# Performance work log

Measured on AMD Instinct MI355X. Metric: run time of the kernel, lower is better.

The kernel has to match this reference:

```python
import jax, jax.numpy as jnp
import numpy as np
import math

B, S, D, H = 4, 2048, 1024, 16
DK = D // H


def setup_inputs() -> dict:
    key = jax.random.key(0)
    ks = jax.random.split(key, 5)
    stdv_in = math.sqrt(3.0 / (2 * D))
    stdv_out = math.sqrt(1.0 / D)
    return {
        "query": jax.random.normal(ks[0], (B, S, D), dtype=jnp.float32),
        "key": jax.random.normal(ks[1], (B, S, D), dtype=jnp.float32),
        "value": jax.random.normal(ks[2], (B, S, D), dtype=jnp.float32),
        "input_weight": jax.random.uniform(ks[3], (3, D, D), dtype=jnp.float32, minval=-stdv_in, maxval=stdv_in),
        "output_weight": jax.random.uniform(ks[4], (D, D), dtype=jnp.float32, minval=-stdv_out, maxval=stdv_out),
    }


def reference(query, key, value, input_weight, output_weight):
    # x @ W.T, split into heads: (B,S,D) -> (B,H,S,dk)
    def proj(x, w):
        return (x @ w.T).reshape(B, S, H, DK).transpose(0, 2, 1, 3)

    q = proj(query, input_weight[0])
    k = proj(key, input_weight[1])
    v = proj(value, input_weight[2])

    scores = jnp.einsum("bhqd,bhkd->bhqk", q, k) / math.sqrt(DK)  # (B,H,S,S)
    similarity = jax.nn.softmax(scores, axis=-1)
    attn = jnp.einsum("bhqk,bhkd->bhqd", similarity, v)  # (B,H,S,dk)
    attn = attn.transpose(0, 2, 1, 3).reshape(B, S, D)
    attn = attn @ output_weight.T
    # mean_simi_across_heads=True default
    sim_mean = jnp.mean(similarity, axis=1)  # (B,S,S)
    return attn, sim_mean
```

## Files before the change

### kernel.cpp

```cpp
#include <hip/hip_runtime.h>

typedef _Float16 f16x8 __attribute__((ext_vector_type(8)));
typedef _Float16 f16x4 __attribute__((ext_vector_type(4)));
typedef _Float16 f16x2 __attribute__((ext_vector_type(2)));
typedef __fp16 h16x2 __attribute__((ext_vector_type(2)));
typedef float f32x4 __attribute__((ext_vector_type(4)));

#define SWB(row, c8) ((((row) << 3) + (((c8) ^ ((row) & 7)))) << 3)

__device__ __forceinline__ float exp2_fast(float x) {
  return __builtin_amdgcn_exp2f(x);
}

__device__ __forceinline__ f16x2 pkrtz(float a, float b) {
  h16x2 r = __builtin_amdgcn_cvt_pkrtz(a, b);
  return *(f16x2*)&r;
}

__device__ __forceinline__ f16x8 pack8(float4 f0, float4 f1) {
  f16x2 p0 = pkrtz(f0.x, f0.y);
  f16x2 p1 = pkrtz(f0.z, f0.w);
  f16x2 p2 = pkrtz(f1.x, f1.y);
  f16x2 p3 = pkrtz(f1.z, f1.w);
  f16x4 a = __builtin_shufflevector(p0, p1, 0, 1, 2, 3);
  f16x4 b = __builtin_shufflevector(p2, p3, 0, 1, 2, 3);
  return __builtin_shufflevector(a, b, 0, 1, 2, 3, 4, 5, 6, 7);
}

#define LOG2E 1.44269504088896340736f

__global__ __launch_bounds__(256) void conv_kernel(
    const float* __restrict__ q, const float* __restrict__ k,
    const float* __restrict__ v, const float* __restrict__ w_in,
    const float* __restrict__ w_out, _Float16* __restrict__ Xc,
    _Float16* __restrict__ W16, float qscale) {
  int t = blockIdx.x * 256 + threadIdx.x;
  if (t < 3145728) {
    int plane = t >> 20, off = t & 1048575;
    const float* src = (plane == 0 ? q : (plane == 1 ? k : v)) + (size_t)off * 8;
    float4 f0 = *(const float4*)src;
    float4 f1 = *(const float4*)(src + 4);
    *(f16x8*)&Xc[(size_t)t * 8] = pack8(f0, f1);
  } else {
    int t2 = t - 3145728;
    int plane = t2 >> 17, off = t2 & 131071;
    const float* src = (plane < 3 ? w_in + (size_t)plane * 1048576 : w_out) + (size_t)off * 8;
    float sc = (plane == 0) ? qscale : 1.0f;
    float4 f0 = *(const float4*)src;
    float4 f1 = *(const float4*)(src + 4);
    f0.x *= sc; f0.y *= sc; f0.z *= sc; f0.w *= sc;
    f1.x *= sc; f1.y *= sc; f1.z *= sc; f1.w *= sc;
    *(f16x8*)&W16[(size_t)t2 * 8] = pack8(f0, f1);
  }
}

template <int EPI>
__global__ __launch_bounds__(256) void gemm_kernel(const _Float16* __restrict__ A0,
                                                   const _Float16* __restrict__ W16,
                                                   void* Oq, void* Ok, void* Ov) {
  __shared__ _Float16 As[128 * 64];
  __shared__ _Float16 Bs[128 * 64];
  const int tid = threadIdx.x;
  const int w = tid >> 6, lane = tid & 63, quad = lane >> 4, l16 = lane & 15;
  const int m0 = blockIdx.y * 128, n0 = blockIdx.x * 128;
  const int z = blockIdx.z;
  const int wm = (w & 1) * 64, wn = (w >> 1) * 64;
  const int srow = tid >> 3, c8 = tid & 7;

  const _Float16* A = (EPI == 0) ? A0 + (size_t)z * 8388608 : A0;
  const _Float16* W = (EPI == 0) ? W16 + (size_t)z * 1048576 : W16 + (size_t)3 * 1048576;

  f32x4 acc[4][4];
#pragma unroll
  for (int i = 0; i < 4; i++)
#pragma unroll
    for (int j = 0; j < 4; j++) acc[i][j] = (f32x4){0.f, 0.f, 0.f, 0.f};

  f16x8 pa[4], pb[4];
#pragma unroll
  for (int u = 0; u < 4; u++) {
    pa[u] = *(const f16x8*)&A[(size_t)(m0 + srow + 32 * u) * 1024 + c8 * 8];
    pb[u] = *(const f16x8*)&W[(size_t)(n0 + srow + 32 * u) * 1024 + c8 * 8];
  }
#pragma unroll
  for (int u = 0; u < 4; u++) {
    *(f16x8*)&As[SWB(srow + 32 * u, c8)] = pa[u];
    *(f16x8*)&Bs[SWB(srow + 32 * u, c8)] = pb[u];
  }

  for (int k0 = 0; k0 < 1024; k0 += 64) {
    __syncthreads();
    if (k0 < 960) {
      int kn = k0 + 64;
#pragma unroll
      for (int u = 0; u < 4; u++) {
        pa[u] = *(const f16x8*)&A[(size_t)(m0 + srow + 32 * u) * 1024 + kn + c8 * 8];
        pb[u] = *(const f16x8*)&W[(size_t)(n0 + srow + 32 * u) * 1024 + kn + c8 * 8];
      }
    }
    f16x8 af[2][4], bf[2][4];
#pragma unroll
    for (int kf = 0; kf < 2; kf++)
#pragma unroll
      for (int i = 0; i < 4; i++) {
        af[kf][i] = *(f16x8*)&As[SWB(wm + i * 16 + l16, kf * 4 + quad)];
        bf[kf][i] = *(f16x8*)&Bs[SWB(wn + i * 16 + l16, kf * 4 + quad)];
      }
#pragma unroll
    for (int kf = 0; kf < 2; kf++)
#pragma unroll
      for (int i = 0; i < 4; i++)
#pragma unroll
        for (int j = 0; j < 4; j++)
          acc[i][j] = __builtin_amdgcn_mfma_f32_16x16x32_f16(af[kf][i], bf[kf][j], acc[i][j], 0, 0, 0);
    __syncthreads();
    if (k0 < 960) {
#pragma unroll
      for (int u = 0; u < 4; u++) {
        *(f16x8*)&As[SWB(srow + 32 * u, c8)] = pa[u];
        *(f16x8*)&Bs[SWB(srow + 32 * u, c8)] = pb[u];
      }
    }
  }

  if (EPI == 1) {
    float* o = (float*)Oq;
#pragma unroll
    for (int i = 0; i < 4; i++)
#pragma unroll
      for (int j = 0; j < 4; j++)
#pragma unroll
        for (int r = 0; r < 4; r++) {
          int mg = m0 + wm + i * 16 + quad * 4 + r;
          int ng = n0 + wn + j * 16 + l16;
          o[(size_t)mg * 1024 + ng] = acc[i][j][r];
        }
  } else {
    _Float16* o = (_Float16*)(z == 0 ? Oq : (z == 1 ? Ok : Ov));
#pragma unroll
    for (int i = 0; i < 4; i++)
#pragma unroll
      for (int j = 0; j < 4; j++) {
        if (z < 2) {
#pragma unroll
          for (int r = 0; r < 4; r++) {
            int mg = m0 + wm + i * 16 + quad * 4 + r;
            int ng = n0 + wn + j * 16 + l16;
            int bb = mg >> 11, ss = mg & 2047, hh = ng >> 6, dd = ng & 63;
            o[((size_t)(bb * 16 + hh) << 17) + ss * 64 + dd] = (_Float16)acc[i][j][r];
          }
        } else {
          int mg0 = m0 + wm + i * 16 + quad * 4;
          int ng = n0 + wn + j * 16 + l16;
          int bb = mg0 >> 11, ss0 = mg0 & 2047, hh = ng >> 6, dd = ng & 63;
          f16x4 pk;
#pragma unroll
          for (int r = 0; r < 4; r++) pk[r] = (_Float16)acc[i][j][r];
          *(f16x4*)&o[((size_t)(bb * 16 + hh) << 17) + (size_t)dd * 2048 + ss0] = pk;
        }
      }
  }
}

__global__ __launch_bounds__(256) void attn_kernel(const _Float16* __restrict__ Q,
                                                   const _Float16* __restrict__ K,
                                                   const _Float16* __restrict__ Vt,
                                                   _Float16* __restrict__ O,
                                                   float* __restrict__ rl) {
  __shared__ _Float16 Kt[64 * 64];
  __shared__ _Float16 Vtt[64 * 64];
  __shared__ _Float16 Pl[128 * 64];
  const int tid = threadIdx.x;
  const int w = tid >> 6, lane = tid & 63, quad = lane >> 4, l16 = lane & 15;
  const int h = blockIdx.y, b = blockIdx.z;
  const size_t base = (size_t)(b * 16 + h) << 17;
  const _Float16* Qh = Q + base;
  const _Float16* Kh = K + base;
  const _Float16* Vth = Vt + base;
  const int q0 = blockIdx.x * 128;
  const int wq = q0 + w * 32;
  const int c0 = tid, c1 = tid + 256;
  const int r0 = c0 >> 3, c80 = c0 & 7, r1 = c1 >> 3, c81 = c1 & 7;

  f16x8 aq[2][2];
#pragma unroll
  for (int i = 0; i < 2; i++)
#pragma unroll
    for (int kf = 0; kf < 2; kf++)
      aq[i][kf] = *(const f16x8*)&Qh[(size_t)(wq + i * 16 + l16) * 64 + kf * 32 + quad * 8];

  f32x4 accO[2][4];
  float lsum[2][4];
#pragma unroll
  for (int i = 0; i < 2; i++)
#pragma unroll
    for (int j = 0; j < 4; j++) {
      accO[i][j] = (f32x4){0.f, 0.f, 0.f, 0.f};
      lsum[i][j] = 0.f;
    }
  const f32x4 zero4 = (f32x4){0.f, 0.f, 0.f, 0.f};

  f16x8 kreg[2], vreg[2];
  kreg[0] = *(const f16x8*)&Kh[(size_t)r0 * 64 + c80 * 8];
  kreg[1] = *(const f16x8*)&Kh[(size_t)r1 * 64 + c81 * 8];
  vreg[0] = *(const f16x8*)&Vth[(size_t)r0 * 2048 + c80 * 8];
  vreg[1] = *(const f16x8*)&Vth[(size_t)r1 * 2048 + c81 * 8];
  *(f16x8*)&Kt[SWB(r0, c80)] = kreg[0];
  *(f16x8*)&Kt[SWB(r1, c81)] = kreg[1];
  *(f16x8*)&Vtt[SWB(r0, c80)] = vreg[0];
  *(f16x8*)&Vtt[SWB(r1, c81)] = vreg[1];

  for (int it = 0; it < 32; it++) {
    __syncthreads();
    if (it < 31) {
      int n0 = (it + 1) * 64;
      kreg[0] = *(const f16x8*)&Kh[(size_t)(n0 + r0) * 64 + c80 * 8];
      kreg[1] = *(const f16x8*)&Kh[(size_t)(n0 + r1) * 64 + c81 * 8];
      vreg[0] = *(const f16x8*)&Vth[(size_t)r0 * 2048 + n0 + c80 * 8];
      vreg[1] = *(const f16x8*)&Vth[(size_t)r1 * 2048 + n0 + c81 * 8];
    }
    f16x8 bk[4][2];
#pragma unroll
    for (int jj = 0; jj < 4; jj++)
#pragma unroll
      for (int kf = 0; kf < 2; kf++)
        bk[jj][kf] = *(f16x8*)&Kt[SWB(jj * 16 + l16, kf * 4 + quad)];
    f32x4 sv[2][4];
#pragma unroll
    for (int i = 0; i < 2; i++)
#pragma unroll
      for (int jj = 0; jj < 4; jj++) {
        f32x4 t = __builtin_amdgcn_mfma_f32_16x16x32_f16(aq[i][0], bk[jj][0], zero4, 0, 0, 0);
        sv[i][jj] = __builtin_amdgcn_mfma_f32_16x16x32_f16(aq[i][1], bk[jj][1], t, 0, 0, 0);
      }
#pragma unroll
    for (int i = 0; i < 2; i++)
#pragma unroll
      for (int jj = 0; jj < 4; jj++)
#pragma unroll
        for (int r = 0; r < 4; r++) {
          float p = exp2_fast(sv[i][jj][r]);
          lsum[i][r] += p;
          int qr = w * 32 + i * 16 + quad * 4 + r;
          int cc = jj * 2 + (l16 >> 3);
          Pl[(qr << 6) + ((cc ^ (qr & 7)) << 3) + (l16 & 7)] = (_Float16)p;
        }
    __asm__ volatile("s_waitcnt lgkmcnt(0)" ::: "memory");
    f16x8 ap[2][2], bv[4][2];
#pragma unroll
    for (int i = 0; i < 2; i++)
#pragma unroll
      for (int kf = 0; kf < 2; kf++)
        ap[i][kf] = *(f16x8*)&Pl[SWB(w * 32 + i * 16 + l16, kf * 4 + quad)];
#pragma unroll
    for (int jd = 0; jd < 4; jd++)
#pragma unroll
      for (int kf = 0; kf < 2; kf++)
        bv[jd][kf] = *(f16x8*)&Vtt[SWB(jd * 16 + l16, kf * 4 + quad)];
#pragma unroll
    for (int i = 0; i < 2; i++)
#pragma unroll
      for (int jd = 0; jd < 4; jd++) {
        accO[i][jd] = __builtin_amdgcn_mfma_f32_16x16x32_f16(ap[i][0], bv[jd][0], accO[i][jd], 0, 0, 0);
        accO[i][jd] = __builtin_amdgcn_mfma_f32_16x16x32_f16(ap[i][1], bv[jd][1], accO[i][jd], 0, 0, 0);
      }
    __syncthreads();
    if (it < 31) {
      *(f16x8*)&Kt[SWB(r0, c80)] = kreg[0];
      *(f16x8*)&Kt[SWB(r1, c81)] = kreg[1];
      *(f16x8*)&Vtt[SWB(r0, c80)] = vreg[0];
      *(f16x8*)&Vtt[SWB(r1, c81)] = vreg[1];
    }
  }

  float rlv[2][4];
#pragma unroll
  for (int i = 0; i < 2; i++)
#pragma unroll
    for (int r = 0; r < 4; r++) {
      float v = lsum[i][r];
      v += __shfl_xor(v, 1);
      v += __shfl_xor(v, 2);
      v += __shfl_xor(v, 4);
      v += __shfl_xor(v, 8);
      rlv[i][r] = 1.0f / v;
    }
  if (l16 == 0) {
#pragma unroll
    for (int i = 0; i < 2; i++)
#pragma unroll
      for (int r = 0; r < 4; r++)
        rl[(b * 16 + h) * 2048 + wq + i * 16 + quad * 4 + r] = rlv[i][r];
  }
#pragma unroll
  for (int i = 0; i < 2; i++)
#pragma unroll
    for (int jd = 0; jd < 4; jd++)
#pragma unroll
      for (int r = 0; r < 4; r++) {
        int rowq = wq + i * 16 + quad * 4 + r;
        O[(size_t)(b * 2048 + rowq) * 1024 + h * 64 + jd * 16 + l16] =
            (_Float16)(accO[i][jd][r] * rlv[i][r]);
      }
}

__global__ __launch_bounds__(512) void sim_kernel(const _Float16* __restrict__ Q,
                                                  const _Float16* __restrict__ K,
                                                  const float* __restrict__ rl,
                                                  float* __restrict__ out) {
  __shared__ _Float16 Ks[128 * 64];
  const int tid = threadIdx.x;
  const int w = tid >> 6, lane = tid & 63, quad = lane >> 4, l16 = lane & 15;
  const int n0 = blockIdx.x * 128, q0 = blockIdx.y * 128, b = blockIdx.z;
  const f32x4 zero4 = (f32x4){0.f, 0.f, 0.f, 0.f};
  const int c0 = tid, c1 = tid + 512;
  const int r0 = c0 >> 3, c80 = c0 & 7, r1 = c1 >> 3, c81 = c1 & 7;

  f32x4 acc[8];
#pragma unroll
  for (int jj = 0; jj < 8; jj++) acc[jj] = (f32x4){0.f, 0.f, 0.f, 0.f};

  f16x8 kreg[2];
  kreg[0] = *(const f16x8*)&K[((size_t)(b * 16) << 17) + (size_t)(n0 + r0) * 64 + c80 * 8];
  kreg[1] = *(const f16x8*)&K[((size_t)(b * 16) << 17) + (size_t)(n0 + r1) * 64 + c81 * 8];
  *(f16x8*)&Ks[SWB(r0, c80)] = kreg[0];
  *(f16x8*)&Ks[SWB(r1, c81)] = kreg[1];

  for (int h = 0; h < 16; h++) {
    __syncthreads();
    if (h < 15) {
      const size_t kb = (size_t)(b * 16 + h + 1) << 17;
      kreg[0] = *(const f16x8*)&K[kb + (size_t)(n0 + r0) * 64 + c80 * 8];
      kreg[1] = *(const f16x8*)&K[kb + (size_t)(n0 + r1) * 64 + c81 * 8];
    }
    const size_t qb = ((size_t)(b * 16 + h) << 17) + (size_t)(q0 + w * 16 + l16) * 64;
    f16x8 aq0 = *(const f16x8*)&Q[qb + quad * 8];
    f16x8 aq1 = *(const f16x8*)&Q[qb + 32 + quad * 8];
    float rv[4];
#pragma unroll
    for (int r = 0; r < 4; r++)
      rv[r] = rl[(b * 16 + h) * 2048 + q0 + w * 16 + quad * 4 + r];
#pragma unroll
    for (int jj = 0; jj < 8; jj++) {
      f16x8 b0 = *(f16x8*)&Ks[SWB(jj * 16 + l16, quad)];
      f16x8 b1 = *(f16x8*)&Ks[SWB(jj * 16 + l16, 4 + quad)];
      f32x4 sv = __builtin_amdgcn_mfma_f32_16x16x32_f16(aq0, b0, zero4, 0, 0, 0);
      sv = __builtin_amdgcn_mfma_f32_16x16x32_f16(aq1, b1, sv, 0, 0, 0);
#pragma unroll
      for (int r = 0; r < 4; r++) acc[jj][r] += exp2_fast(sv[r]) * rv[r];
    }
    __syncthreads();
    if (h < 15) {
      *(f16x8*)&Ks[SWB(r0, c80)] = kreg[0];
      *(f16x8*)&Ks[SWB(r1, c81)] = kreg[1];
    }
  }
#pragma unroll
  for (int jj = 0; jj < 8; jj++)
#pragma unroll
    for (int r = 0; r < 4; r++) {
      int rowq = q0 + w * 16 + quad * 4 + r;
      out[(size_t)(b * 2048 + rowq) * 2048 + n0 + jj * 16 + l16] = acc[jj][r] * 0.0625f;
    }
}

extern "C" void kernel_launch(void* const* d_in, const int* in_sizes, int n_in,
                              void* d_out, int out_size, void* d_ws, size_t ws_size,
                              hipStream_t stream) {
  const float* q = (const float*)d_in[0];
  const float* k = (const float*)d_in[1];
  const float* v = (const float*)d_in[2];
  const float* w_in = (const float*)d_in[3];
  const float* w_out = (const float*)d_in[4];

  _Float16* Qw = (_Float16*)d_ws;
  _Float16* Kw = Qw + 8388608;
  _Float16* Vt = Kw + 8388608;
  _Float16* Ow = Vt + 8388608;
  float* rlw = (float*)(Ow + 8388608);

  float* out_attn = (float*)d_out;
  float* out_sim = out_attn + 8388608;
  _Float16* Xc = (_Float16*)out_sim;
  _Float16* W16 = Xc + 3 * 8388608;

  conv_kernel<<<14336, 256, 0, stream>>>(q, k, v, w_in, w_out, Xc, W16,
                                         0.125f * LOG2E);
  gemm_kernel<0><<<dim3(8, 64, 3), 256, 0, stream>>>(Xc, W16, Qw, Kw, Vt);
  attn_kernel<<<dim3(16, 16, 4), 256, 0, stream>>>(Qw, Kw, Vt, Ow, rlw);
  gemm_kernel<1><<<dim3(8, 64, 1), 256, 0, stream>>>(Ow, W16, out_attn, nullptr, nullptr);
  sim_kernel<<<dim3(16, 16, 4), 512, 0, stream>>>(Qw, Kw, rlw, out_sim);
}
```

Before: 487.4 us.

## Keep softmax probabilities in registers by computing transposed S tile

The QK^T MFMA operands are swapped so each lane holds the score fragment in the layout needed as the A operand of the PV MFMA, and the probabilities are packed straight into registers instead of going through a shared-memory P buffer. To match the new k-ordering, the V tile is stored into shared memory with a permuted half-chunk layout. Row sums are now reduced across quads instead of within 16 lanes. This removes a per-iteration LDS write/read round trip and its wait, at the cost of split 4-element LDS stores for V.

```diff
diff --git a/kernel.cpp b/kernel.cpp
--- a/kernel.cpp
+++ b/kernel.cpp
@@ -169,7 +169,6 @@
                                                    float* __restrict__ rl) {
   __shared__ _Float16 Kt[64 * 64];
   __shared__ _Float16 Vtt[64 * 64];
-  __shared__ _Float16 Pl[128 * 64];
   const int tid = threadIdx.x;
   const int w = tid >> 6, lane = tid & 63, quad = lane >> 4, l16 = lane & 15;
   const int h = blockIdx.y, b = blockIdx.z;
@@ -181,6 +180,8 @@
   const int wq = q0 + w * 32;
   const int c0 = tid, c1 = tid + 256;
   const int r0 = c0 >> 3, c80 = c0 & 7, r1 = c1 >> 3, c81 = c1 & 7;
+  const int vA0 = (c80 >> 2) * 4 + (c80 & 1) * 2, vh0 = ((c80 >> 1) & 1) * 4;
+  const int vA1 = (c81 >> 2) * 4 + (c81 & 1) * 2, vh1 = ((c81 >> 1) & 1) * 4;
 
   f16x8 aq[2][2];
 #pragma unroll
@@ -190,14 +191,13 @@
       aq[i][kf] = *(const f16x8*)&Qh[(size_t)(wq + i * 16 + l16) * 64 + kf * 32 + quad * 8];
 
   f32x4 accO[2][4];
-  float lsum[2][4];
-#pragma unroll
-  for (int i = 0; i < 2; i++)
-#pragma unroll
-    for (int j = 0; j < 4; j++) {
-      accO[i][j] = (f32x4){0.f, 0.f, 0.f, 0.f};
-      lsum[i][j] = 0.f;
-    }
+  float lsum[2];
+#pragma unroll
+  for (int i = 0; i < 2; i++) {
+    lsum[i] = 0.f;
+#pragma unroll
+    for (int j = 0; j < 4; j++) accO[i][j] = (f32x4){0.f, 0.f, 0.f, 0.f};
+  }
   const f32x4 zero4 = (f32x4){0.f, 0.f, 0.f, 0.f};
 
   f16x8 kreg[2], vreg[2];
@@ -207,8 +207,16 @@
   vreg[1] = *(const f16x8*)&Vth[(size_t)r1 * 2048 + c81 * 8];
   *(f16x8*)&Kt[SWB(r0, c80)] = kreg[0];
   *(f16x8*)&Kt[SWB(r1, c81)] = kreg[1];
-  *(f16x8*)&Vtt[SWB(r0, c80)] = vreg[0];
-  *(f16x8*)&Vtt[SWB(r1, c81)] = vreg[1];
+  {
+    f16x4 lo0 = __builtin_shufflevector(vreg[0], vreg[0], 0, 1, 2, 3);
+    f16x4 hi0 = __builtin_shufflevector(vreg[0], vreg[0], 4, 5, 6, 7);
+    *(f16x4*)&Vtt[SWB(r0, vA0) + vh0] = lo0;
+    *(f16x4*)&Vtt[SWB(r0, vA0 + 1) + vh0] = hi0;
+    f16x4 lo1 = __builtin_shufflevector(vreg[1], vreg[1], 0, 1, 2, 3);
+    f16x4 hi1 = __builtin_shufflevector(vreg[1], vreg[1], 4, 5, 6, 7);
+    *(f16x4*)&Vtt[SWB(r1, vA1) + vh1] = lo1;
+    *(f16x4*)&Vtt[SWB(r1, vA1 + 1) + vh1] = hi1;
+  }
 
   for (int it = 0; it < 32; it++) {
     __syncthreads();
@@ -230,28 +238,23 @@
     for (int i = 0; i < 2; i++)
 #pragma unroll
       for (int jj = 0; jj < 4; jj++) {
-        f32x4 t = __builtin_amdgcn_mfma_f32_16x16x32_f16(aq[i][0], bk[jj][0], zero4, 0, 0, 0);
-        sv[i][jj] = __builtin_amdgcn_mfma_f32_16x16x32_f16(aq[i][1], bk[jj][1], t, 0, 0, 0);
-      }
+        f32x4 t = __builtin_amdgcn_mfma_f32_16x16x32_f16(bk[jj][0], aq[i][0], zero4, 0, 0, 0);
+        sv[i][jj] = __builtin_amdgcn_mfma_f32_16x16x32_f16(bk[jj][1], aq[i][1], t, 0, 0, 0);
+      }
+    f16x8 ap[2][2];
 #pragma unroll
     for (int i = 0; i < 2; i++)
 #pragma unroll
-      for (int jj = 0; jj < 4; jj++)
-#pragma unroll
-        for (int r = 0; r < 4; r++) {
-          float p = exp2_fast(sv[i][jj][r]);
-          lsum[i][r] += p;
-          int qr = w * 32 + i * 16 + quad * 4 + r;
-          int cc = jj * 2 + (l16 >> 3);
-          Pl[(qr << 6) + ((cc ^ (qr & 7)) << 3) + (l16 & 7)] = (_Float16)p;
-        }
-    __asm__ volatile("s_waitcnt lgkmcnt(0)" ::: "memory");
-    f16x8 ap[2][2], bv[4][2];
-#pragma unroll
-    for (int i = 0; i < 2; i++)
-#pragma unroll
       for (int kf = 0; kf < 2; kf++)
-        ap[i][kf] = *(f16x8*)&Pl[SWB(w * 32 + i * 16 + l16, kf * 4 + quad)];
+#pragma unroll
+        for (int hi = 0; hi < 2; hi++)
+#pragma unroll
+          for (int r = 0; r < 4; r++) {
+            float p = exp2_fast(sv[i][2 * kf + hi][r]);
+            lsum[i] += p;
+            ap[i][kf][hi * 4 + r] = (_Float16)p;
+          }
+    f16x8 bv[4][2];
 #pragma unroll
     for (int jd = 0; jd < 4; jd++)
 #pragma unroll
@@ -268,30 +271,37 @@
     if (it < 31) {
       *(f16x8*)&Kt[SWB(r0, c80)] = kreg[0];
       *(f16x8*)&Kt[SWB(r1, c81)] = kreg[1];
-      *(f16x8*)&Vtt[SWB(r0, c80)] = vreg[0];
-      *(f16x8*)&Vtt[SWB(r1, c81)] = vreg[1];
-    }
-  }
-
-  float rlv[2][4];
+      f16x4 lo0 = __builtin_shufflevector(vreg[0], vreg[0], 0, 1, 2, 3);
+      f16x4 hi0 = __builtin_shufflevector(vreg[0], vreg[0], 4, 5, 6, 7);
+      *(f16x4*)&Vtt[SWB(r0, vA0) + vh0] = lo0;
+      *(f16x4*)&Vtt[SWB(r0, vA0 + 1) + vh0] = hi0;
+      f16x4 lo1 = __builtin_shufflevector(vreg[1], vreg[1], 0, 1, 2, 3);
+      f16x4 hi1 = __builtin_shufflevector(vreg[1], vreg[1], 4, 5, 6, 7);
+      *(f16x4*)&Vtt[SWB(r1, vA1) + vh1] = lo1;
+      *(f16x4*)&Vtt[SWB(r1, vA1 + 1) + vh1] = hi1;
+    }
+  }
+
+  float rinv[2];
+#pragma unroll
+  for (int i = 0; i < 2; i++) {
+    float v = lsum[i];
+    v += __shfl_xor(v, 16);
+    v += __shfl_xor(v, 32);
+    rinv[i] = 1.0f / v;
+  }
+  if (lane < 16) {
+#pragma unroll
+    for (int i = 0; i < 2; i++)
+      rl[(b * 16 + h) * 2048 + wq + i * 16 + lane] = rinv[i];
+  }
+  float rO[2][4];
 #pragma unroll
   for (int i = 0; i < 2; i++)
 #pragma unroll
-    for (int r = 0; r < 4; r++) {
-      float v = lsum[i][r];
-      v += __shfl_xor(v, 1);
-      v += __shfl_xor(v, 2);
-      v += __shfl_xor(v, 4);
-      v += __shfl_xor(v, 8);
-      rlv[i][r] = 1.0f / v;
-    }
-  if (l16 == 0) {
-#pragma unroll
-    for (int i = 0; i < 2; i++)
-#pragma unroll
-      for (int r = 0; r < 4; r++)
-        rl[(b * 16 + h) * 2048 + wq + i * 16 + quad * 4 + r] = rlv[i][r];
-  }
+    for (int r = 0; r < 4; r++)
+      rO[i][r] = __shfl(rinv[i], quad * 4 + r);
+
 #pragma unroll
   for (int i = 0; i < 2; i++)
 #pragma unroll
@@ -300,7 +310,7 @@
       for (int r = 0; r < 4; r++) {
         int rowq = wq + i * 16 + quad * 4 + r;
         O[(size_t)(b * 2048 + rowq) * 1024 + h * 64 + jd * 16 + l16] =
-            (_Float16)(accO[i][jd][r] * rlv[i][r]);
+            (_Float16)(accO[i][jd][r] * rO[i][r]);
       }
 }
 
```

After: 468.3 us. -3.9%, faster.
